# Optimization experiments

Measured on AMD Instinct MI355X. Metric: run time of the kernel, lower is better.

## Reference

```python
import jax, jax.numpy as jnp
import numpy as np

F_IN = 10000
M = 3
CARD = 5
LOG_2PI = float(np.log(2.0 * np.pi))


def _normal_logprob(x, means, stds):
    # x: [N, F, 1]; means/stds: [1, F, M] -> [N, F, M]
    z = (x - means) / stds
    return -0.5 * (z * z) - jnp.log(stds) - 0.5 * LOG_2PI


def _sum_layer(x, w):
    # x: [N, F, Cin]; w: [F, Cin, Cout] -> [N, F, Cout]
    logw = jax.nn.log_softmax(w, axis=1)
    return jax.scipy.special.logsumexp(x[:, :, :, None] + logw[None], axis=2)


def _product_layer(x, card):
    # log-domain product = segmented sum over blocks of `card` features
    n, f, c = x.shape
    return x.reshape(n, f // card, card, c).sum(axis=2)


def setup_inputs() -> dict:
    key = jax.random.key(0)
    ks = jax.random.split(key, 9)
    x = jax.random.normal(ks[0], (4096, F_IN), dtype=jnp.float32)
    means = jax.random.normal(ks[1], (1, F_IN, M), dtype=jnp.float32)
    stds = jax.random.uniform(ks[2], (1, F_IN, M), dtype=jnp.float32, minval=0.5, maxval=1.5)
    w1 = jax.random.normal(ks[3], (F_IN, M, 1), dtype=jnp.float32)
    w2 = jax.random.normal(ks[4], (F_IN // 5, 1, 1), dtype=jnp.float32)
    w3 = jax.random.normal(ks[5], (F_IN // 25, 1, 1), dtype=jnp.float32)
    w4 = jax.random.normal(ks[6], (F_IN // 125, 1, 1), dtype=jnp.float32)
    w5 = jax.random.normal(ks[7], (F_IN // 625, 1, 1), dtype=jnp.float32)
    rand_idxs = jax.random.permutation(ks[8], F_IN).astype(jnp.int32)
    return {"x": x, "means": means, "stds": stds, "w1": w1, "w2": w2,
            "w3": w3, "w4": w4, "w5": w5, "rand_idxs": rand_idxs}


def reference(x, means, stds, w1, w2, w3, w4, w5, rand_idxs):
    # scope permutation gather
    xp = x[:, rand_idxs]                          # [N, F]
    y = _normal_logprob(xp[:, :, None], means, stds)  # [N, F, M]
    y = _sum_layer(y, w1)                          # [N, F, 1]
    y = _product_layer(y, CARD)                    # [N, F/5, 1]
    y = _sum_layer(y, w2)
    y = _product_layer(y, CARD)                    # [N, F/25, 1]
    y = _sum_layer(y, w3)
    y = _product_layer(y, CARD)                    # [N, F/125, 1]
    y = _sum_layer(y, w4)
    y = _product_layer(y, CARD)                    # [N, F/625, 1]
    y = _sum_layer(y, w5)
    y = _product_layer(y, F_IN // 5 ** 4)          # [N, 1, 1]
    return y
```

## Files before the change

kernel.cpp:

```cpp
#include <hip/hip_runtime.h>
#include <math.h>

#define F_IN 10000
#define NROWS 4096
#define CGROUPS 8
#define CH_PER_CG 5
#define BLK 512
#define RPW 4
#define PASSES 2
#define ROWBLOCKS 64

typedef float v4f __attribute__((ext_vector_type(4)));

__device__ __forceinline__ v4f ntload4(const float* p) {
    return __builtin_nontemporal_load((const v4f*)p);
}

__global__ void spn_prep_kernel(const float* __restrict__ means,
                                const float* __restrict__ stds,
                                const float* __restrict__ w1,
                                const int* __restrict__ rand_idxs,
                                float* __restrict__ ws,
                                float* __restrict__ out) {
    int f = blockIdx.x * blockDim.x + threadIdx.x;
    if (f < NROWS) out[f] = 0.0f;
    if (f >= F_IN) return;

    int j = rand_idxs[f];

    float wa = w1[f * 3 + 0];
    float wb = w1[f * 3 + 1];
    float wc = w1[f * 3 + 2];
    float wm = fmaxf(fmaxf(wa, wb), wc);
    float lse = wm + __logf(__expf(wa - wm) + __expf(wb - wm) + __expf(wc - wm));

    const float INV_SQRT2 = 0.70710678118654752440f;
    const float HALF_LOG_2PI = 0.91893853320467274178f;

#pragma unroll
    for (int m = 0; m < 3; m++) {
        float w  = w1[f * 3 + m] - lse;
        float sd = stds[f * 3 + m];
        float mu = means[f * 3 + m];
        float a  = INV_SQRT2 / sd;
        float b  = -mu * a;
        float c  = w - __logf(sd) - HALF_LOG_2PI;
        ws[(0 + m) * F_IN + j] = a;
        ws[(3 + m) * F_IN + j] = b;
        ws[(6 + m) * F_IN + j] = c;
    }
}

__device__ __forceinline__ void col_term(float xv,
                                         float a0, float b0, float c0,
                                         float a1, float b1, float c1,
                                         float a2, float b2, float c2,
                                         float& mx_out, float& s_out) {
    float u0 = fmaf(xv, a0, b0);
    float u1 = fmaf(xv, a1, b1);
    float u2 = fmaf(xv, a2, b2);
    float v0 = fmaf(-u0, u0, c0);
    float v1 = fmaf(-u1, u1, c1);
    float v2 = fmaf(-u2, u2, c2);
    float mx = fmaxf(fmaxf(v0, v1), v2);
    float me = __builtin_amdgcn_fmed3f(v0, v1, v2);
    float mn = fminf(fminf(v0, v1), v2);
    float s  = 1.0f + __expf(me - mx) + __expf(mn - mx);
    mx_out = mx;
    s_out  = s;
}

__global__ __launch_bounds__(BLK) void spn_main_kernel(const float* __restrict__ x,
                                                       const float* __restrict__ ws,
                                                       float* __restrict__ out) {
    __shared__ v4f ldsbuf[CH_PER_CG * 9 * 64];

    const int tid  = threadIdx.x;
    const int wave = tid >> 6;
    const int lane = tid & 63;
    const int rb   = blockIdx.x >> 3;
    const int cg   = blockIdx.x & 7;

    const v4f* wsv = (const v4f*)ws;
    for (int i = tid; i < CH_PER_CG * 9 * 64; i += BLK) {
        int it  = i / (9 * 64);
        int rem = i - it * (9 * 64);
        int a   = rem >> 6;
        int v   = rem & 63;
        int col = (cg + it * 8) * 256 + v * 4;
        v4f val = (v4f)(0.0f);
        if (col < F_IN) val = wsv[a * (F_IN / 4) + (col >> 2)];
        ldsbuf[i] = val;
    }
    __syncthreads();

    for (int g = 0; g < PASSES; ++g) {
        const int row0 = rb * 64 + g * 32 + wave * RPW;
        const float* xr0 = x + (size_t)row0 * F_IN;

        float accm[RPW], prod[RPW];
#pragma unroll
        for (int r = 0; r < RPW; r++) { accm[r] = 0.0f; prod[r] = 1.0f; }

        v4f xv[RPW];
        {
            int jc = cg * 256 + lane * 4;
#pragma unroll
            for (int r = 0; r < RPW; r++)
                xv[r] = ntload4(xr0 + (size_t)r * F_IN + jc);
        }

#pragma unroll
        for (int it = 0; it < CH_PER_CG; ++it) {
            const int c = cg + it * 8;
            const int jcur = c * 256 + lane * 4;
            const bool vcur = (jcur < F_IN);

            v4f xn[RPW];
            if (it < CH_PER_CG - 1) {
                int jn = (c + 8) * 256 + lane * 4;
                int jnc = (jn < F_IN) ? jn : 0;
#pragma unroll
                for (int r = 0; r < RPW; r++)
                    xn[r] = ntload4(xr0 + (size_t)r * F_IN + jnc);
            }

            const v4f* Lp = ldsbuf + it * (9 * 64);
            const v4f A0 = Lp[0 * 64 + lane];
            const v4f A1 = Lp[1 * 64 + lane];
            const v4f A2 = Lp[2 * 64 + lane];
            const v4f B0 = Lp[3 * 64 + lane];
            const v4f B1 = Lp[4 * 64 + lane];
            const v4f B2 = Lp[5 * 64 + lane];
            const v4f C0 = Lp[6 * 64 + lane];
            const v4f C1 = Lp[7 * 64 + lane];
            const v4f C2 = Lp[8 * 64 + lane];

#pragma unroll
            for (int r = 0; r < RPW; r++) {
                float m0, s0, m1, s1, m2, s2, m3, s3;
                col_term(xv[r].x, A0.x, B0.x, C0.x, A1.x, B1.x, C1.x, A2.x, B2.x, C2.x, m0, s0);
                col_term(xv[r].y, A0.y, B0.y, C0.y, A1.y, B1.y, C1.y, A2.y, B2.y, C2.y, m1, s1);
                col_term(xv[r].z, A0.z, B0.z, C0.z, A1.z, B1.z, C1.z, A2.z, B2.z, C2.z, m2, s2);
                col_term(xv[r].w, A0.w, B0.w, C0.w, A1.w, B1.w, C1.w, A2.w, B2.w, C2.w, m3, s3);

                float smx = (m0 + m1) + (m2 + m3);
                float sp  = (s0 * s1) * (s2 * s3);
                accm[r] += vcur ? smx : 0.0f;
                prod[r] *= vcur ? sp : 1.0f;
            }

            if (it < CH_PER_CG - 1) {
#pragma unroll
                for (int r = 0; r < RPW; r++) xv[r] = xn[r];
            }
        }

#pragma unroll
        for (int r = 0; r < RPW; r++) {
            float part = accm[r] + __logf(prod[r]);
#pragma unroll
            for (int off = 32; off > 0; off >>= 1)
                part += __shfl_xor(part, off, 64);
            if (lane == 0)
                atomicAdd(&out[row0 + r], part);
        }
    }
}

extern "C" void kernel_launch(void* const* d_in, const int* in_sizes, int n_in,
                              void* d_out, int out_size, void* d_ws, size_t ws_size,
                              hipStream_t stream) {
    const float* x         = (const float*)d_in[0];
    const float* means     = (const float*)d_in[1];
    const float* stds      = (const float*)d_in[2];
    const float* w1        = (const float*)d_in[3];
    const int*   rand_idxs = (const int*)d_in[8];

    float* out = (float*)d_out;
    float* ws  = (float*)d_ws;

    spn_prep_kernel<<<(F_IN + 255) / 256, 256, 0, stream>>>(means, stds, w1, rand_idxs, ws, out);

    spn_main_kernel<<<ROWBLOCKS * CGROUPS, BLK, 0, stream>>>(x, ws, out);
}
```

Before: 254.0 us.

## Drop LDS parameter staging and regrid main kernel into smaller blocks

New measurement: 271.9 us. 7.0% more time.

```diff
diff --git a/kernel.cpp b/kernel.cpp
--- a/kernel.cpp
+++ b/kernel.cpp
@@ -3,12 +3,10 @@
 
 #define F_IN 10000
 #define NROWS 4096
-#define CGROUPS 8
-#define CH_PER_CG 5
-#define BLK 512
+#define CGROUPS 4
+#define CH_PER_CG 10
 #define RPW 4
-#define PASSES 2
-#define ROWBLOCKS 64
+#define ROWBLOCKS 256
 
 typedef float v4f __attribute__((ext_vector_type(4)));
 
@@ -70,101 +68,82 @@
     s_out  = s;
 }
 
-__global__ __launch_bounds__(BLK) void spn_main_kernel(const float* __restrict__ x,
+__global__ __launch_bounds__(256) void spn_main_kernel(const float* __restrict__ x,
                                                        const float* __restrict__ ws,
                                                        float* __restrict__ out) {
-    __shared__ v4f ldsbuf[CH_PER_CG * 9 * 64];
+    const int wave = threadIdx.x >> 6;
+    const int lane = threadIdx.x & 63;
+    const int rb   = blockIdx.x >> 2;
+    const int cg   = blockIdx.x & 3;
+    const int row0 = rb * 16 + wave * RPW;
+    const float* xr0 = x + (size_t)row0 * F_IN;
 
-    const int tid  = threadIdx.x;
-    const int wave = tid >> 6;
-    const int lane = tid & 63;
-    const int rb   = blockIdx.x >> 3;
-    const int cg   = blockIdx.x & 7;
+    float accm[RPW], prod[RPW];
+#pragma unroll
+    for (int r = 0; r < RPW; r++) { accm[r] = 0.0f; prod[r] = 1.0f; }
 
-    const v4f* wsv = (const v4f*)ws;
-    for (int i = tid; i < CH_PER_CG * 9 * 64; i += BLK) {
-        int it  = i / (9 * 64);
-        int rem = i - it * (9 * 64);
-        int a   = rem >> 6;
-        int v   = rem & 63;
-        int col = (cg + it * 8) * 256 + v * 4;
-        v4f val = (v4f)(0.0f);
-        if (col < F_IN) val = wsv[a * (F_IN / 4) + (col >> 2)];
-        ldsbuf[i] = val;
+    v4f xv[RPW];
+    {
+        int jc = cg * 256 + lane * 4;
+#pragma unroll
+        for (int r = 0; r < RPW; r++)
+            xv[r] = ntload4(xr0 + (size_t)r * F_IN + jc);
     }
-    __syncthreads();
 
-    for (int g = 0; g < PASSES; ++g) {
-        const int row0 = rb * 64 + g * 32 + wave * RPW;
-        const float* xr0 = x + (size_t)row0 * F_IN;
+#pragma unroll
+    for (int it = 0; it < CH_PER_CG; ++it) {
+        const int c = cg + it * 4;
+        const int jcur = c * 256 + lane * 4;
+        const bool vcur = (jcur < F_IN);
+        const int q = vcur ? (jcur >> 2) : 0;
 
-        float accm[RPW], prod[RPW];
-#pragma unroll
-        for (int r = 0; r < RPW; r++) { accm[r] = 0.0f; prod[r] = 1.0f; }
+        const v4f A0 = ((const v4f*)(ws + 0 * F_IN))[q];
+        const v4f A1 = ((const v4f*)(ws + 1 * F_IN))[q];
+        const v4f A2 = ((const v4f*)(ws + 2 * F_IN))[q];
+        const v4f B0 = ((const v4f*)(ws + 3 * F_IN))[q];
+        const v4f B1 = ((const v4f*)(ws + 4 * F_IN))[q];
+        const v4f B2 = ((const v4f*)(ws + 5 * F_IN))[q];
+        const v4f C0 = ((const v4f*)(ws + 6 * F_IN))[q];
+        const v4f C1 = ((const v4f*)(ws + 7 * F_IN))[q];
+        const v4f C2 = ((const v4f*)(ws + 8 * F_IN))[q];
 
-        v4f xv[RPW];
-        {
-            int jc = cg * 256 + lane * 4;
+        v4f xn[RPW];
+        if (it < CH_PER_CG - 1) {
+            int jn = (c + 4) * 256 + lane * 4;
+            int jnc = (jn < F_IN) ? jn : 0;
 #pragma unroll
             for (int r = 0; r < RPW; r++)
-                xv[r] = ntload4(xr0 + (size_t)r * F_IN + jc);
-        }
-
-#pragma unroll
-        for (int it = 0; it < CH_PER_CG; ++it) {
-            const int c = cg + it * 8;
-            const int jcur = c * 256 + lane * 4;
-            const bool vcur = (jcur < F_IN);
-
-            v4f xn[RPW];
-            if (it < CH_PER_CG - 1) {
-                int jn = (c + 8) * 256 + lane * 4;
-                int jnc = (jn < F_IN) ? jn : 0;
-#pragma unroll
-                for (int r = 0; r < RPW; r++)
-                    xn[r] = ntload4(xr0 + (size_t)r * F_IN + jnc);
-            }
-
-            const v4f* Lp = ldsbuf + it * (9 * 64);
-            const v4f A0 = Lp[0 * 64 + lane];
-            const v4f A1 = Lp[1 * 64 + lane];
-            const v4f A2 = Lp[2 * 64 + lane];
-            const v4f B0 = Lp[3 * 64 + lane];
-            const v4f B1 = Lp[4 * 64 + lane];
-            const v4f B2 = Lp[5 * 64 + lane];
-            const v4f C0 = Lp[6 * 64 + lane];
-            const v4f C1 = Lp[7 * 64 + lane];
-            const v4f C2 = Lp[8 * 64 + lane];
-
-#pragma unroll
-            for (int r = 0; r < RPW; r++) {
-                float m0, s0, m1, s1, m2, s2, m3, s3;
-                col_term(xv[r].x, A0.x, B0.x, C0.x, A1.x, B1.x, C1.x, A2.x, B2.x, C2.x, m0, s0);
-                col_term(xv[r].y, A0.y, B0.y, C0.y, A1.y, B1.y, C1.y, A2.y, B2.y, C2.y, m1, s1);
-                col_term(xv[r].z, A0.z, B0.z, C0.z, A1.z, B1.z, C1.z, A2.z, B2.z, C2.z, m2, s2);
-                col_term(xv[r].w, A0.w, B0.w, C0.w, A1.w, B1.w, C1.w, A2.w, B2.w, C2.w, m3, s3);
-
-                float smx = (m0 + m1) + (m2 + m3);
-                float sp  = (s0 * s1) * (s2 * s3);
-                accm[r] += vcur ? smx : 0.0f;
-                prod[r] *= vcur ? sp : 1.0f;
-            }
-
-            if (it < CH_PER_CG - 1) {
-#pragma unroll
-                for (int r = 0; r < RPW; r++) xv[r] = xn[r];
-            }
+                xn[r] = ntload4(xr0 + (size_t)r * F_IN + jnc);
         }
 
 #pragma unroll
         for (int r = 0; r < RPW; r++) {
-            float part = accm[r] + __logf(prod[r]);
+            float m0, s0, m1, s1, m2, s2, m3, s3;
+            col_term(xv[r].x, A0.x, B0.x, C0.x, A1.x, B1.x, C1.x, A2.x, B2.x, C2.x, m0, s0);
+            col_term(xv[r].y, A0.y, B0.y, C0.y, A1.y, B1.y, C1.y, A2.y, B2.y, C2.y, m1, s1);
+            col_term(xv[r].z, A0.z, B0.z, C0.z, A1.z, B1.z, C1.z, A2.z, B2.z, C2.z, m2, s2);
+            col_term(xv[r].w, A0.w, B0.w, C0.w, A1.w, B1.w, C1.w, A2.w, B2.w, C2.w, m3, s3);
+
+            float smx = (m0 + m1) + (m2 + m3);
+            float sp  = (s0 * s1) * (s2 * s3);
+            accm[r] += vcur ? smx : 0.0f;
+            prod[r] *= vcur ? sp : 1.0f;
+        }
+
+        if (it < CH_PER_CG - 1) {
 #pragma unroll
-            for (int off = 32; off > 0; off >>= 1)
-                part += __shfl_xor(part, off, 64);
-            if (lane == 0)
-                atomicAdd(&out[row0 + r], part);
+            for (int r = 0; r < RPW; r++) xv[r] = xn[r];
         }
+    }
+
+#pragma unroll
+    for (int r = 0; r < RPW; r++) {
+        float part = accm[r] + __logf(prod[r]);
+#pragma unroll
+        for (int off = 32; off > 0; off >>= 1)
+            part += __shfl_xor(part, off, 64);
+        if (lane == 0)
+            atomicAdd(&out[row0 + r], part);
     }
 }
 
@@ -182,5 +161,5 @@
 
     spn_prep_kernel<<<(F_IN + 255) / 256, 256, 0, stream>>>(means, stds, w1, rand_idxs, ws, out);
 
-    spn_main_kernel<<<ROWBLOCKS * CGROUPS, BLK, 0, stream>>>(x, ws, out);
+    spn_main_kernel<<<ROWBLOCKS * CGROUPS, 256, 0, stream>>>(x, ws, out);
 }
```
